# Kernel optimization log

Measured on AMD Instinct MI355X. Metric: run time of the kernel, lower is better.

Reference implementation:

```python
import jax, jax.numpy as jnp
import numpy as np

RES = 128            # occupancy grid resolution per axis
HIDDEN = 128         # MLP width
PE_POS = 10          # positional-encoding freqs for xyz
PE_DIR = 4           # positional-encoding freqs for viewdirs
S_MAX = 192          # max marching steps per ray
STEP = 0.027         # render_step_size (~aabb diagonal / S_MAX)
ERT = 1e-4           # early_stop_eps (transmittance threshold)
AABB_MIN = -1.5
AABB_MAX = 1.5
WHITE_BKGD = 1.0     # white_bkgd=True


def _posenc(x, L):
    # x: [..., 3] -> [..., 3 + 6L]
    freqs = 2.0 ** jnp.arange(L, dtype=x.dtype)
    xb = x[..., None, :] * freqs[:, None]                 # [..., L, 3]
    enc = jnp.concatenate([jnp.sin(xb), jnp.cos(xb)], axis=-1)  # [..., L, 6]
    return jnp.concatenate([x, enc.reshape(x.shape[:-1] + (-1,))], axis=-1)


def setup_inputs() -> dict:
    key = jax.random.key(0)
    ks = jax.random.split(key, 8)
    B, N = 1, 2048
    # camera origins on a sphere of radius 2.5 outside the aabb, rays aimed near the center
    o = jax.random.normal(ks[0], (B, N, 3), dtype=jnp.float32)
    o = o / jnp.linalg.norm(o, axis=-1, keepdims=True) * 2.5
    target = jax.random.normal(ks[1], (B, N, 3), dtype=jnp.float32) * 0.3
    d = target - o
    d = d / jnp.linalg.norm(d, axis=-1, keepdims=True)
    occ_grid = jax.random.bernoulli(ks[2], 0.3, (RES, RES, RES))
    din_pos = 3 + 6 * PE_POS   # 63
    din_dir = 3 + 6 * PE_DIR   # 27
    sc = lambda n: 1.0 / np.sqrt(n)
    W0 = jax.random.normal(ks[3], (din_pos, HIDDEN), dtype=jnp.float32) * sc(din_pos)
    W1 = jax.random.normal(ks[4], (HIDDEN, HIDDEN), dtype=jnp.float32) * sc(HIDDEN)
    w_sigma = jax.random.normal(ks[5], (HIDDEN, 1), dtype=jnp.float32) * sc(HIDDEN)
    W2 = jax.random.normal(ks[6], (HIDDEN + din_dir, HIDDEN), dtype=jnp.float32) * sc(HIDDEN)
    w_rgb = jax.random.normal(ks[7], (HIDDEN, 3), dtype=jnp.float32) * sc(HIDDEN)
    return {"rays_o": o, "viewdirs": d, "occ_grid": occ_grid,
            "W0": W0, "W1": W1, "w_sigma": w_sigma, "W2": W2, "w_rgb": w_rgb}


def reference(rays_o, viewdirs, occ_grid, W0, W1, w_sigma, W2, w_rgb):
    B, N, _ = rays_o.shape
    o = rays_o.reshape(-1, 3)          # [R, 3]
    d = viewdirs.reshape(-1, 3)        # [R, 3]
    R = o.shape[0]
    # ray / aabb intersection
    inv_d = 1.0 / jnp.where(jnp.abs(d) < 1e-9, 1e-9, d)
    t0 = (AABB_MIN - o) * inv_d
    t1 = (AABB_MAX - o) * inv_d
    t_near = jnp.maximum(jnp.max(jnp.minimum(t0, t1), axis=-1), 0.0)  # [R]
    t_far = jnp.min(jnp.maximum(t0, t1), axis=-1)                     # [R]
    # fixed-step marching (padded to S_MAX, masked) == nerfacc sampling with occ grid
    i = jnp.arange(S_MAX, dtype=rays_o.dtype)
    t_start = t_near[:, None] + STEP * i[None, :]   # [R, S]
    t_end = t_start + STEP
    t_mid = t_start + 0.5 * STEP
    inside = (t_mid < t_far[:, None]) & ((t_far > t_near)[:, None])
    pts = o[:, None, :] + d[:, None, :] * t_mid[..., None]  # [R, S, 3]
    # occupancy lookup (skip empty cells)
    gidx = jnp.clip(((pts - AABB_MIN) / (AABB_MAX - AABB_MIN) * RES).astype(jnp.int32), 0, RES - 1)
    occ = occ_grid[gidx[..., 0], gidx[..., 1], gidx[..., 2]]  # [R, S] bool
    mask = inside & occ
    # NeRF MLP (rgb_alpha_fn): sigma from pos, rgb from pos feature + viewdir
    pe_p = _posenc(pts.reshape(-1, 3), PE_POS)                               # [RS, 63]
    pe_d = _posenc(jnp.broadcast_to(d[:, None, :], pts.shape).reshape(-1, 3), PE_DIR)  # [RS, 27]
    h = jax.nn.relu(pe_p @ W0)
    h = jax.nn.relu(h @ W1)
    sigma = (h @ w_sigma).reshape(R, S_MAX)
    h2 = jax.nn.relu(jnp.concatenate([h, pe_d], axis=-1) @ W2)
    rgb = jax.nn.sigmoid(h2 @ w_rgb).reshape(R, S_MAX, 3)
    # alpha compositing (nerfacc.rendering) with early termination
    delta = t_end - t_start
    alpha = (1.0 - jnp.exp(-jax.nn.relu(sigma) * delta)) * mask.astype(sigma.dtype)
    trans = jnp.cumprod(1.0 - alpha + 1e-10, axis=-1)
    T = jnp.concatenate([jnp.ones((R, 1), alpha.dtype), trans[:, :-1]], axis=-1)  # exclusive
    T = T * (T > ERT).astype(T.dtype)  # early ray termination
    w = T * alpha                      # [R, S]
    rgb_map = jnp.einsum('rs,rsc->rc', w, rgb)
    opacity = jnp.sum(w, axis=-1, keepdims=True)
    depth = jnp.sum(w * t_mid, axis=-1, keepdims=True)
    rgb_map = rgb_map + (1.0 - opacity) * WHITE_BKGD
    return (rgb_map.reshape(B, N, 3), depth.reshape(B, N, 1), opacity.reshape(B, N, 1))
```

## Files before the change

### kernel.cpp

```cpp
#include <hip/hip_runtime.h>
#include <stdint.h>

#define NRAYS 2048
#define SMAX  192
#define RESG  128
#define STEPF 0.027f
#define ERTF  1e-4f
#define CAP   (NRAYS * SMAX)

typedef __attribute__((ext_vector_type(8)))  short bf16x8;
typedef __attribute__((ext_vector_type(16))) float f32x16;

__device__ __forceinline__ uint32_t f2b(float x) {
    uint32_t u = __builtin_bit_cast(uint32_t, x);
    return (u + 0x7fffu + ((u >> 16) & 1u)) >> 16;
}
__device__ __forceinline__ uint32_t bpack(float lo, float hi) {
    return f2b(lo) | (f2b(hi) << 16);
}

__device__ __forceinline__ void ray_aabb(float ox, float oy, float oz,
                                         float dx, float dy, float dz,
                                         float& tn, float& tf) {
    float ix = 1.0f / ((fabsf(dx) < 1e-9f) ? 1e-9f : dx);
    float iy = 1.0f / ((fabsf(dy) < 1e-9f) ? 1e-9f : dy);
    float iz = 1.0f / ((fabsf(dz) < 1e-9f) ? 1e-9f : dz);
    float t0x = (-1.5f - ox) * ix, t1x = (1.5f - ox) * ix;
    float t0y = (-1.5f - oy) * iy, t1y = (1.5f - oy) * iy;
    float t0z = (-1.5f - oz) * iz, t1z = (1.5f - oz) * iz;
    float tnx = fminf(t0x, t1x), tfx = fmaxf(t0x, t1x);
    float tny = fminf(t0y, t1y), tfy = fmaxf(t0y, t1y);
    float tnz = fminf(t0z, t1z), tfz = fmaxf(t0z, t1z);
    tn = fmaxf(fmaxf(fmaxf(tnx, tny), tnz), 0.0f);
    tf = fminf(fminf(tfx, tfy), tfz);
}

__global__ void k_prep(const float* __restrict__ W0, const float* __restrict__ W1,
                       const float* __restrict__ W2, uint32_t* __restrict__ wf) {
    int b = blockIdx.x;
    int g = b >> 2, oc = b & 3;
    int lane = threadIdx.x;
    int out = oc * 32 + (lane & 31);
    const float* W; int kbase, Klim;
    if (g < 4)       { W = W0; kbase = g * 16;        Klim = 63;  }
    else if (g < 12) { W = W1; kbase = (g - 4) * 16;  Klim = 128; }
    else             { W = W2; kbase = (g - 12) * 16; Klim = 155; }
    uint32_t d[4];
    #pragma unroll
    for (int h = 0; h < 4; ++h) {
        int k0 = kbase + ((lane >> 5) << 3) + h * 2;
        float lo = (k0     < Klim) ? W[(size_t)k0 * 128 + out]       : 0.0f;
        float hi = (k0 + 1 < Klim) ? W[(size_t)(k0 + 1) * 128 + out] : 0.0f;
        d[h] = bpack(lo, hi);
    }
    ((uint4*)wf)[b * 64 + lane] = make_uint4(d[0], d[1], d[2], d[3]);
}

__global__ __launch_bounds__(256) void k_count(
        const float* __restrict__ ro, const float* __restrict__ rd,
        const int* __restrict__ occ,
        int* __restrict__ rayCount, unsigned long long* __restrict__ masks) {
    int r = blockIdx.x * 4 + (threadIdx.x >> 6);
    int lane = threadIdx.x & 63;
    float ox = ro[r*3+0], oy = ro[r*3+1], oz = ro[r*3+2];
    float dx = rd[r*3+0], dy = rd[r*3+1], dz = rd[r*3+2];
    float tn, tf;
    ray_aabb(ox, oy, oz, dx, dy, dz, tn, tf);
    int cnt = 0;
    #pragma unroll
    for (int c = 0; c < 3; ++c) {
        int s = c * 64 + lane;
        float t_mid = (tn + STEPF * (float)s) + 0.5f * STEPF;
        bool inside = (t_mid < tf) && (tf > tn);
        bool act = false;
        if (inside) {
            float px = ox + dx * t_mid;
            float py = oy + dy * t_mid;
            float pz = oz + dz * t_mid;
            int gx = min(max((int)((px + 1.5f) / 3.0f * 128.0f), 0), RESG - 1);
            int gy = min(max((int)((py + 1.5f) / 3.0f * 128.0f), 0), RESG - 1);
            int gz = min(max((int)((pz + 1.5f) / 3.0f * 128.0f), 0), RESG - 1);
            act = occ[(gx * RESG + gy) * RESG + gz] != 0;
        }
        unsigned long long mb = __ballot(act);
        if (lane == 0) masks[r * 3 + c] = mb;
        cnt += __popcll(mb);
    }
    if (lane == 0) rayCount[r] = cnt;
}

__global__ __launch_bounds__(1024) void k_scan(
        const int* __restrict__ rayCount, int* __restrict__ rayOff,
        int* __restrict__ cnt_total) {
    __shared__ int wsum[16];
    int tid = threadIdx.x;
    int a = rayCount[2 * tid], b = rayCount[2 * tid + 1];
    int s = a + b;
    int lane = tid & 63, w = tid >> 6;
    int v = s;
    #pragma unroll
    for (int off = 1; off < 64; off <<= 1) {
        int t = __shfl_up(v, off);
        if (lane >= off) v += t;
    }
    if (lane == 63) wsum[w] = v;
    __syncthreads();
    if (tid < 16) {
        int x = wsum[tid];
        #pragma unroll
        for (int off = 1; off < 16; off <<= 1) {
            int t = __shfl_up(x, off, 16);
            if (tid >= off) x += t;
        }
        wsum[tid] = x;
    }
    __syncthreads();
    int wbase = (w == 0) ? 0 : wsum[w - 1];
    int incl = wbase + v;
    int excl = incl - s;
    rayOff[2 * tid]     = excl;
    rayOff[2 * tid + 1] = excl + a;
    if (tid == 1023) cnt_total[0] = incl;
}

__global__ __launch_bounds__(256) void k_fill(
        const float* __restrict__ ro, const float* __restrict__ rd,
        const int* __restrict__ rayOff, const unsigned long long* __restrict__ masks,
        int2* __restrict__ ids, float4* __restrict__ pos) {
    int r = blockIdx.x * 4 + (threadIdx.x >> 6);
    int lane = threadIdx.x & 63;
    float ox = ro[r*3+0], oy = ro[r*3+1], oz = ro[r*3+2];
    float dx = rd[r*3+0], dy = rd[r*3+1], dz = rd[r*3+2];
    float tn, tf;
    ray_aabb(ox, oy, oz, dx, dy, dz, tn, tf);
    int base = rayOff[r];
    #pragma unroll
    for (int c = 0; c < 3; ++c) {
        unsigned long long m = masks[r * 3 + c];
        if ((m >> lane) & 1ull) {
            int within = __popcll(m & ((1ull << lane) - 1ull));
            int s = c * 64 + lane;
            float t_mid = (tn + STEPF * (float)s) + 0.5f * STEPF;
            float px = ox + dx * t_mid;
            float py = oy + dy * t_mid;
            float pz = oz + dz * t_mid;
            ids[base + within] = make_int2(r, s);
            pos[base + within] = make_float4(px, py, pz, t_mid);
        }
        base += __popcll(m);
    }
}

__global__ __launch_bounds__(512) void k_mlp(
        const uint32_t* __restrict__ wfrag, const float* __restrict__ wsig,
        const float* __restrict__ wrgb, const float* __restrict__ vd,
        const int* __restrict__ cnt, const int2* __restrict__ ids,
        const float4* __restrict__ pos, float4* __restrict__ rgba) {
    __shared__ __align__(16) short actA[64 * 128];
    __shared__ __align__(16) short bufB[64 * 256];
    __shared__ float4 sPos[64];
    __shared__ int    sRay[64];
    __shared__ float  sV[128];
    __shared__ float  sR[384];

    const int tid  = threadIdx.x;
    const int wave = tid >> 6;
    const int lane = tid & 63;
    const int oc   = wave & 3;
    const int sc   = wave >> 2;
    const int lo5  = lane & 31;
    const int hi5  = lane >> 5;

    if (tid < 128) sV[tid] = wsig[tid];
    if (tid >= 128 && tid < 512) sR[tid - 128] = wrgb[tid - 128];

    bf16x8 wf[22];
    {
        const uint4* src = (const uint4*)wfrag;
        #pragma unroll
        for (int g = 0; g < 22; ++g) {
            uint4 v = src[(g * 4 + oc) * 64 + lane];
            wf[g] = __builtin_bit_cast(bf16x8, v);
        }
    }

    const int total  = *cnt;
    const int ntiles = (total + 63) >> 6;
    const int mrow   = sc * 32 + lo5;
    const int rswz   = (mrow & 15) << 4;

    for (int t = blockIdx.x; t < ntiles; t += gridDim.x) {
        const int base = t << 6;
        __syncthreads();
        if (tid < 64) {
            int gi = base + tid;
            if (gi < total) { sRay[tid] = ids[gi].x; sPos[tid] = pos[gi]; }
            else            { sRay[tid] = 0; sPos[tid] = make_float4(0.f,0.f,0.f,0.f); }
        }
        __syncthreads();

        {
            int m = tid >> 3, p = tid & 7;
            float4 P = sPos[m];
            int swz = (m & 15) << 4;
            uint32_t dw[4];
            #pragma unroll
            for (int jp = 0; jp < 4; ++jp) {
                float v[2];
                #pragma unroll
                for (int q = 0; q < 2; ++q) {
                    int c = p * 8 + jp * 2 + q;
                    float val;
                    if (c < 3)        val = (c == 0) ? P.x : ((c == 1) ? P.y : P.z);
                    else if (c >= 63) val = 0.0f;
                    else {
                        int cc = c - 3, l = cc / 6, jj = cc - 6 * l;
                        int a3 = (jj >= 3) ? jj - 3 : jj;
                        float comp = (a3 == 0) ? P.x : ((a3 == 1) ? P.y : P.z);
                        float arg = comp * (float)(1 << l);
                        val = (jj < 3) ? __sinf(arg) : __cosf(arg);
                    }
                    v[q] = val;
                }
                dw[jp] = bpack(v[0], v[1]);
            }
            *(uint4*)((char*)actA + m * 256 + ((p * 16) ^ swz)) = make_uint4(dw[0], dw[1], dw[2], dw[3]);
            if (p < 4) {
                int ray = sRay[m];
                float Dx = vd[ray*3+0], Dy = vd[ray*3+1], Dz = vd[ray*3+2];
                #pragma unroll
                for (int jp = 0; jp < 4; ++jp) {
                    float v[2];
                    #pragma unroll
                    for (int q = 0; q < 2; ++q) {
                        int c = p * 8 + jp * 2 + q;
                        float val;
                        if (c < 3)        val = (c == 0) ? Dx : ((c == 1) ? Dy : Dz);
                        else if (c >= 27) val = 0.0f;
                        else {
                            int cc = c - 3, l = cc / 6, jj = cc - 6 * l;
                            int a3 = (jj >= 3) ? jj - 3 : jj;
                            float comp = (a3 == 0) ? Dx : ((a3 == 1) ? Dy : Dz);
                            float arg = comp * (float)(1 << l);
                            val = (jj < 3) ? __sinf(arg) : __cosf(arg);
                        }
                        v[q] = val;
                    }
                    dw[jp] = bpack(v[0], v[1]);
                }
                *(uint4*)((char*)bufB + m * 512 + ((256 + p * 16) ^ swz)) = make_uint4(dw[0], dw[1], dw[2], dw[3]);
            }
        }
        __syncthreads();

        {
            f32x16 acc = {};
            #pragma unroll
            for (int kb = 0; kb < 4; ++kb) {
                bf16x8 bf = *(const bf16x8*)((const char*)actA + mrow * 256 + ((kb * 32 + (hi5 << 4)) ^ rswz));
                acc = __builtin_amdgcn_mfma_f32_32x32x16_bf16(wf[kb], bf, acc, 0, 0, 0);
            }
            #pragma unroll
            for (int g = 0; g < 4; ++g) {
                int outb = (oc * 32 + g * 8 + (hi5 << 2)) * 2;
                uint32_t d0 = bpack(fmaxf(acc[g*4+0], 0.f), fmaxf(acc[g*4+1], 0.f));
                uint32_t d1 = bpack(fmaxf(acc[g*4+2], 0.f), fmaxf(acc[g*4+3], 0.f));
                *(uint2*)((char*)bufB + mrow * 512 + (outb ^ rswz)) = make_uint2(d0, d1);
            }
        }
        __syncthreads();

        {
            f32x16 acc = {};
            #pragma unroll
            for (int kb = 0; kb < 8; ++kb) {
                bf16x8 bf = *(const bf16x8*)((const char*)bufB + mrow * 512 + ((kb * 32 + (hi5 << 4)) ^ rswz));
                acc = __builtin_amdgcn_mfma_f32_32x32x16_bf16(wf[4 + kb], bf, acc, 0, 0, 0);
            }
            #pragma unroll
            for (int g = 0; g < 4; ++g) {
                int outb = (oc * 32 + g * 8 + (hi5 << 2)) * 2;
                uint32_t d0 = bpack(fmaxf(acc[g*4+0], 0.f), fmaxf(acc[g*4+1], 0.f));
                uint32_t d1 = bpack(fmaxf(acc[g*4+2], 0.f), fmaxf(acc[g*4+3], 0.f));
                *(uint2*)((char*)actA + mrow * 256 + (outb ^ rswz)) = make_uint2(d0, d1);
            }
        }
        __syncthreads();

        {
            f32x16 acc = {};
            #pragma unroll
            for (int kb = 0; kb < 8; ++kb) {
                bf16x8 bf = *(const bf16x8*)((const char*)actA + mrow * 256 + ((kb * 32 + (hi5 << 4)) ^ rswz));
                acc = __builtin_amdgcn_mfma_f32_32x32x16_bf16(wf[12 + kb], bf, acc, 0, 0, 0);
            }
            #pragma unroll
            for (int kb = 8; kb < 10; ++kb) {
                bf16x8 bf = *(const bf16x8*)((const char*)bufB + mrow * 512 + ((kb * 32 + (hi5 << 4)) ^ rswz));
                acc = __builtin_amdgcn_mfma_f32_32x32x16_bf16(wf[12 + kb], bf, acc, 0, 0, 0);
            }
            #pragma unroll
            for (int g = 0; g < 4; ++g) {
                int outb = (oc * 32 + g * 8 + (hi5 << 2)) * 2;
                uint32_t d0 = bpack(fmaxf(acc[g*4+0], 0.f), fmaxf(acc[g*4+1], 0.f));
                uint32_t d1 = bpack(fmaxf(acc[g*4+2], 0.f), fmaxf(acc[g*4+3], 0.f));
                *(uint2*)((char*)bufB + mrow * 512 + (outb ^ rswz)) = make_uint2(d0, d1);
            }
        }
        __syncthreads();

        {
            int m = tid >> 3, p = tid & 7;
            int swz = (m & 15) << 4;
            float sp = 0.f, r0 = 0.f, r1 = 0.f, r2 = 0.f;
            #pragma unroll
            for (int hh = 0; hh < 2; ++hh) {
                uint4 q = *(const uint4*)((const char*)actA + m * 256 + ((p * 32 + hh * 16) ^ swz));
                uint32_t w[4] = {q.x, q.y, q.z, q.w};
                #pragma unroll
                for (int e = 0; e < 4; ++e) {
                    int j = p * 16 + hh * 8 + e * 2;
                    float a0 = __builtin_bit_cast(float, w[e] << 16);
                    float a1 = __builtin_bit_cast(float, w[e] & 0xffff0000u);
                    sp = fmaf(a0, sV[j], sp);
                    sp = fmaf(a1, sV[j + 1], sp);
                }
            }
            #pragma unroll
            for (int hh = 0; hh < 2; ++hh) {
                uint4 q = *(const uint4*)((const char*)bufB + m * 512 + ((p * 32 + hh * 16) ^ swz));
                uint32_t w[4] = {q.x, q.y, q.z, q.w};
                #pragma unroll
                for (int e = 0; e < 4; ++e) {
                    int j = p * 16 + hh * 8 + e * 2;
                    float a0 = __builtin_bit_cast(float, w[e] << 16);
                    float a1 = __builtin_bit_cast(float, w[e] & 0xffff0000u);
                    r0 = fmaf(a0, sR[j*3+0], r0); r1 = fmaf(a0, sR[j*3+1], r1); r2 = fmaf(a0, sR[j*3+2], r2);
                    r0 = fmaf(a1, sR[(j+1)*3+0], r0); r1 = fmaf(a1, sR[(j+1)*3+1], r1); r2 = fmaf(a1, sR[(j+1)*3+2], r2);
                }
            }
            #pragma unroll
            for (int off = 1; off < 8; off <<= 1) {
                sp += __shfl_xor(sp, off);
                r0 += __shfl_xor(r0, off);
                r1 += __shfl_xor(r1, off);
                r2 += __shfl_xor(r2, off);
            }
            if (p == 0 && (base + m) < total) {
                float alpha = 1.0f - __expf(-fmaxf(sp, 0.0f) * STEPF);
                float c0 = 1.0f / (1.0f + __expf(-r0));
                float c1 = 1.0f / (1.0f + __expf(-r1));
                float c2 = 1.0f / (1.0f + __expf(-r2));
                rgba[base + m] = make_float4(c0, c1, c2, alpha);
            }
        }
    }
}

__global__ __launch_bounds__(256) void k_render(
        const int* __restrict__ rayOff, const int* __restrict__ rayCount,
        const float4* __restrict__ rgba, const float* __restrict__ posw,
        float* __restrict__ out) {
    int r = blockIdx.x * 4 + (threadIdx.x >> 6);
    int lane = threadIdx.x & 63;
    int off = rayOff[r], cnt = rayCount[r];
    float T_run = 1.0f;
    float cr = 0.f, cg = 0.f, cb = 0.f, opa = 0.f, dep = 0.f;
    for (int j = 0; j < cnt; j += 64) {
        int idx = j + lane;
        float4 f = make_float4(0.f, 0.f, 0.f, 0.f);
        float tmid = 0.f;
        if (idx < cnt) {
            f = rgba[off + idx];
            tmid = posw[(size_t)(off + idx) * 4 + 3];
        }
        float p = (1.0f - f.w) + 1e-10f;
        #pragma unroll
        for (int o = 1; o < 64; o <<= 1) {
            float v = __shfl_up(p, o);
            if (lane >= o) p *= v;
        }
        float pprev = __shfl_up(p, 1);
        float Texc = (lane == 0) ? T_run : T_run * pprev;
        Texc = (Texc > ERTF) ? Texc : 0.0f;
        float w = Texc * f.w;
        cr += w * f.x; cg += w * f.y; cb += w * f.z;
        opa += w; dep += w * tmid;
        T_run *= __shfl(p, 63);
        if (T_run <= ERTF) break;
    }
    #pragma unroll
    for (int o = 32; o; o >>= 1) {
        cr  += __shfl_xor(cr, o);
        cg  += __shfl_xor(cg, o);
        cb  += __shfl_xor(cb, o);
        opa += __shfl_xor(opa, o);
        dep += __shfl_xor(dep, o);
    }
    if (lane == 0) {
        out[r * 3 + 0] = cr + (1.0f - opa);
        out[r * 3 + 1] = cg + (1.0f - opa);
        out[r * 3 + 2] = cb + (1.0f - opa);
        out[NRAYS * 3 + r] = dep;
        out[NRAYS * 4 + r] = opa;
    }
}

extern "C" void kernel_launch(void* const* d_in, const int* in_sizes, int n_in,
                              void* d_out, int out_size, void* d_ws, size_t ws_size,
                              hipStream_t stream) {
    const float* ro   = (const float*)d_in[0];
    const float* rd   = (const float*)d_in[1];
    const int*   occ  = (const int*)d_in[2];
    const float* W0   = (const float*)d_in[3];
    const float* W1   = (const float*)d_in[4];
    const float* wsig = (const float*)d_in[5];
    const float* W2   = (const float*)d_in[6];
    const float* wrgb = (const float*)d_in[7];
    float* out = (float*)d_out;

    char* ws = (char*)d_ws;
    int*                cnt_total = (int*)ws;
    int*                rayCount  = (int*)(ws + 16);
    int*                rayOff    = (int*)(ws + 8208);
    unsigned long long* masks     = (unsigned long long*)(ws + 16400);
    int2*               ids       = (int2*)(ws + 65552);
    float4*             pos       = (float4*)(ws + 65552 + (size_t)CAP * 8);
    float4*             rgba      = (float4*)(ws + 65552 + (size_t)CAP * 24);
    uint32_t*           wfrag     = (uint32_t*)(ws + 65552 + (size_t)CAP * 40);

    k_prep  <<<88, 64, 0, stream>>>(W0, W1, W2, wfrag);
    k_count <<<NRAYS / 4, 256, 0, stream>>>(ro, rd, occ, rayCount, masks);
    k_scan  <<<1, 1024, 0, stream>>>(rayCount, rayOff, cnt_total);
    k_fill  <<<NRAYS / 4, 256, 0, stream>>>(ro, rd, rayOff, masks, ids, pos);
    k_mlp   <<<1024, 512, 0, stream>>>(wfrag, wsig, wrgb, rd, cnt_total, ids, pos, rgba);
    k_render<<<NRAYS / 4, 256, 0, stream>>>(rayOff, rayCount, rgba, (const float*)pos, out);
}
```

Measured before the change: 119.6 us.

## Enlarge MLP tile to 128 samples, merge weight prep into count kernel

The MLP kernel now processes 128 samples per tile instead of 64. Each wave issues two MFMAs per weight fragment, so every register-resident weight is reused across twice as many rows, and the grid drops from 1024 to 256 blocks. The weight-packing kernel is merged into the count kernel as extra blocks to remove one launch, and the sample id buffer shrinks from int2 to a single int. The trade-off is that LDS use per block roughly doubles, which may lower occupancy, and with fewer, larger tiles the load may balance less evenly across CUs.

```diff
diff --git a/kernel.cpp b/kernel.cpp
--- a/kernel.cpp
+++ b/kernel.cpp
@@ -35,32 +35,36 @@
     tf = fminf(fminf(tfx, tfy), tfz);
 }
 
-__global__ void k_prep(const float* __restrict__ W0, const float* __restrict__ W1,
-                       const float* __restrict__ W2, uint32_t* __restrict__ wf) {
-    int b = blockIdx.x;
-    int g = b >> 2, oc = b & 3;
-    int lane = threadIdx.x;
-    int out = oc * 32 + (lane & 31);
-    const float* W; int kbase, Klim;
-    if (g < 4)       { W = W0; kbase = g * 16;        Klim = 63;  }
-    else if (g < 12) { W = W1; kbase = (g - 4) * 16;  Klim = 128; }
-    else             { W = W2; kbase = (g - 12) * 16; Klim = 155; }
-    uint32_t d[4];
-    #pragma unroll
-    for (int h = 0; h < 4; ++h) {
-        int k0 = kbase + ((lane >> 5) << 3) + h * 2;
-        float lo = (k0     < Klim) ? W[(size_t)k0 * 128 + out]       : 0.0f;
-        float hi = (k0 + 1 < Klim) ? W[(size_t)(k0 + 1) * 128 + out] : 0.0f;
-        d[h] = bpack(lo, hi);
-    }
-    ((uint4*)wf)[b * 64 + lane] = make_uint4(d[0], d[1], d[2], d[3]);
-}
-
-__global__ __launch_bounds__(256) void k_count(
+__global__ __launch_bounds__(256) void k_count_prep(
         const float* __restrict__ ro, const float* __restrict__ rd,
         const int* __restrict__ occ,
-        int* __restrict__ rayCount, unsigned long long* __restrict__ masks) {
-    int r = blockIdx.x * 4 + (threadIdx.x >> 6);
+        const float* __restrict__ W0, const float* __restrict__ W1,
+        const float* __restrict__ W2,
+        int* __restrict__ rayCount, unsigned long long* __restrict__ masks,
+        uint32_t* __restrict__ wfrag) {
+    int b = blockIdx.x;
+    if (b >= NRAYS / 4) {
+        int pb = b - NRAYS / 4;
+        int lane = threadIdx.x;
+        if (lane >= 64) return;
+        int g = pb >> 2, oc = pb & 3;
+        int out = oc * 32 + (lane & 31);
+        const float* W; int kbase, Klim;
+        if (g < 4)       { W = W0; kbase = g * 16;        Klim = 63;  }
+        else if (g < 12) { W = W1; kbase = (g - 4) * 16;  Klim = 128; }
+        else             { W = W2; kbase = (g - 12) * 16; Klim = 155; }
+        uint32_t d[4];
+        #pragma unroll
+        for (int h = 0; h < 4; ++h) {
+            int k0 = kbase + ((lane >> 5) << 3) + h * 2;
+            float lo = (k0     < Klim) ? W[(size_t)k0 * 128 + out]       : 0.0f;
+            float hi = (k0 + 1 < Klim) ? W[(size_t)(k0 + 1) * 128 + out] : 0.0f;
+            d[h] = bpack(lo, hi);
+        }
+        ((uint4*)wfrag)[pb * 64 + lane] = make_uint4(d[0], d[1], d[2], d[3]);
+        return;
+    }
+    int r = b * 4 + (threadIdx.x >> 6);
     int lane = threadIdx.x & 63;
     float ox = ro[r*3+0], oy = ro[r*3+1], oz = ro[r*3+2];
     float dx = rd[r*3+0], dy = rd[r*3+1], dz = rd[r*3+2];
@@ -126,7 +130,7 @@
 __global__ __launch_bounds__(256) void k_fill(
         const float* __restrict__ ro, const float* __restrict__ rd,
         const int* __restrict__ rayOff, const unsigned long long* __restrict__ masks,
-        int2* __restrict__ ids, float4* __restrict__ pos) {
+        int* __restrict__ rayid, float4* __restrict__ pos) {
     int r = blockIdx.x * 4 + (threadIdx.x >> 6);
     int lane = threadIdx.x & 63;
     float ox = ro[r*3+0], oy = ro[r*3+1], oz = ro[r*3+2];
@@ -144,7 +148,7 @@
             float px = ox + dx * t_mid;
             float py = oy + dy * t_mid;
             float pz = oz + dz * t_mid;
-            ids[base + within] = make_int2(r, s);
+            rayid[base + within] = r;
             pos[base + within] = make_float4(px, py, pz, t_mid);
         }
         base += __popcll(m);
@@ -154,12 +158,12 @@
 __global__ __launch_bounds__(512) void k_mlp(
         const uint32_t* __restrict__ wfrag, const float* __restrict__ wsig,
         const float* __restrict__ wrgb, const float* __restrict__ vd,
-        const int* __restrict__ cnt, const int2* __restrict__ ids,
+        const int* __restrict__ cnt, const int* __restrict__ rayid,
         const float4* __restrict__ pos, float4* __restrict__ rgba) {
-    __shared__ __align__(16) short actA[64 * 128];
-    __shared__ __align__(16) short bufB[64 * 256];
-    __shared__ float4 sPos[64];
-    __shared__ int    sRay[64];
+    __shared__ __align__(16) short actA[128 * 128];
+    __shared__ __align__(16) short bufB[128 * 256];
+    __shared__ float4 sPos[128];
+    __shared__ int    sRay[128];
     __shared__ float  sV[128];
     __shared__ float  sR[384];
 
@@ -185,49 +189,53 @@
     }
 
     const int total  = *cnt;
-    const int ntiles = (total + 63) >> 6;
-    const int mrow   = sc * 32 + lo5;
+    const int ntiles = (total + 127) >> 7;
+    const int mrow   = sc * 64 + lo5;
     const int rswz   = (mrow & 15) << 4;
 
     for (int t = blockIdx.x; t < ntiles; t += gridDim.x) {
-        const int base = t << 6;
-        __syncthreads();
-        if (tid < 64) {
+        const int base = t << 7;
+        __syncthreads();
+        if (tid < 128) {
             int gi = base + tid;
-            if (gi < total) { sRay[tid] = ids[gi].x; sPos[tid] = pos[gi]; }
+            if (gi < total) { sRay[tid] = rayid[gi]; sPos[tid] = pos[gi]; }
             else            { sRay[tid] = 0; sPos[tid] = make_float4(0.f,0.f,0.f,0.f); }
         }
         __syncthreads();
 
         {
-            int m = tid >> 3, p = tid & 7;
+            int m = tid >> 2, p = tid & 3;
             float4 P = sPos[m];
             int swz = (m & 15) << 4;
-            uint32_t dw[4];
-            #pragma unroll
-            for (int jp = 0; jp < 4; ++jp) {
-                float v[2];
+            #pragma unroll
+            for (int half = 0; half < 2; ++half) {
+                uint32_t dw[4];
                 #pragma unroll
-                for (int q = 0; q < 2; ++q) {
-                    int c = p * 8 + jp * 2 + q;
-                    float val;
-                    if (c < 3)        val = (c == 0) ? P.x : ((c == 1) ? P.y : P.z);
-                    else if (c >= 63) val = 0.0f;
-                    else {
-                        int cc = c - 3, l = cc / 6, jj = cc - 6 * l;
-                        int a3 = (jj >= 3) ? jj - 3 : jj;
-                        float comp = (a3 == 0) ? P.x : ((a3 == 1) ? P.y : P.z);
-                        float arg = comp * (float)(1 << l);
-                        val = (jj < 3) ? __sinf(arg) : __cosf(arg);
+                for (int jp = 0; jp < 4; ++jp) {
+                    float v[2];
+                    #pragma unroll
+                    for (int q = 0; q < 2; ++q) {
+                        int c = p * 16 + half * 8 + jp * 2 + q;
+                        float val;
+                        if (c < 3)        val = (c == 0) ? P.x : ((c == 1) ? P.y : P.z);
+                        else if (c >= 63) val = 0.0f;
+                        else {
+                            int cc = c - 3, l = cc / 6, jj = cc - 6 * l;
+                            int a3 = (jj >= 3) ? jj - 3 : jj;
+                            float comp = (a3 == 0) ? P.x : ((a3 == 1) ? P.y : P.z);
+                            float arg = comp * (float)(1 << l);
+                            val = (jj < 3) ? __sinf(arg) : __cosf(arg);
+                        }
+                        v[q] = val;
                     }
-                    v[q] = val;
+                    dw[jp] = bpack(v[0], v[1]);
                 }
-                dw[jp] = bpack(v[0], v[1]);
-            }
-            *(uint4*)((char*)actA + m * 256 + ((p * 16) ^ swz)) = make_uint4(dw[0], dw[1], dw[2], dw[3]);
-            if (p < 4) {
+                *(uint4*)((char*)actA + m * 256 + ((p * 32 + half * 16) ^ swz)) = make_uint4(dw[0], dw[1], dw[2], dw[3]);
+            }
+            {
                 int ray = sRay[m];
                 float Dx = vd[ray*3+0], Dy = vd[ray*3+1], Dz = vd[ray*3+2];
+                uint32_t dw[4];
                 #pragma unroll
                 for (int jp = 0; jp < 4; ++jp) {
                     float v[2];
@@ -254,72 +262,93 @@
         __syncthreads();
 
         {
-            f32x16 acc = {};
+            f32x16 a0 = {}, a1 = {};
             #pragma unroll
             for (int kb = 0; kb < 4; ++kb) {
-                bf16x8 bf = *(const bf16x8*)((const char*)actA + mrow * 256 + ((kb * 32 + (hi5 << 4)) ^ rswz));
-                acc = __builtin_amdgcn_mfma_f32_32x32x16_bf16(wf[kb], bf, acc, 0, 0, 0);
+                int cb = (kb * 32 + (hi5 << 4)) ^ rswz;
+                bf16x8 b0 = *(const bf16x8*)((const char*)actA + mrow * 256 + cb);
+                bf16x8 b1 = *(const bf16x8*)((const char*)actA + (mrow + 32) * 256 + cb);
+                a0 = __builtin_amdgcn_mfma_f32_32x32x16_bf16(wf[kb], b0, a0, 0, 0, 0);
+                a1 = __builtin_amdgcn_mfma_f32_32x32x16_bf16(wf[kb], b1, a1, 0, 0, 0);
             }
             #pragma unroll
             for (int g = 0; g < 4; ++g) {
                 int outb = (oc * 32 + g * 8 + (hi5 << 2)) * 2;
-                uint32_t d0 = bpack(fmaxf(acc[g*4+0], 0.f), fmaxf(acc[g*4+1], 0.f));
-                uint32_t d1 = bpack(fmaxf(acc[g*4+2], 0.f), fmaxf(acc[g*4+3], 0.f));
-                *(uint2*)((char*)bufB + mrow * 512 + (outb ^ rswz)) = make_uint2(d0, d1);
+                *(uint2*)((char*)bufB + mrow * 512 + (outb ^ rswz)) =
+                    make_uint2(bpack(fmaxf(a0[g*4+0],0.f), fmaxf(a0[g*4+1],0.f)),
+                               bpack(fmaxf(a0[g*4+2],0.f), fmaxf(a0[g*4+3],0.f)));
+                *(uint2*)((char*)bufB + (mrow + 32) * 512 + (outb ^ rswz)) =
+                    make_uint2(bpack(fmaxf(a1[g*4+0],0.f), fmaxf(a1[g*4+1],0.f)),
+                               bpack(fmaxf(a1[g*4+2],0.f), fmaxf(a1[g*4+3],0.f)));
             }
         }
         __syncthreads();
 
         {
-            f32x16 acc = {};
+            f32x16 a0 = {}, a1 = {};
             #pragma unroll
             for (int kb = 0; kb < 8; ++kb) {
-                bf16x8 bf = *(const bf16x8*)((const char*)bufB + mrow * 512 + ((kb * 32 + (hi5 << 4)) ^ rswz));
-                acc = __builtin_amdgcn_mfma_f32_32x32x16_bf16(wf[4 + kb], bf, acc, 0, 0, 0);
+                int cb = (kb * 32 + (hi5 << 4)) ^ rswz;
+                bf16x8 b0 = *(const bf16x8*)((const char*)bufB + mrow * 512 + cb);
+                bf16x8 b1 = *(const bf16x8*)((const char*)bufB + (mrow + 32) * 512 + cb);
+                a0 = __builtin_amdgcn_mfma_f32_32x32x16_bf16(wf[4 + kb], b0, a0, 0, 0, 0);
+                a1 = __builtin_amdgcn_mfma_f32_32x32x16_bf16(wf[4 + kb], b1, a1, 0, 0, 0);
             }
             #pragma unroll
             for (int g = 0; g < 4; ++g) {
                 int outb = (oc * 32 + g * 8 + (hi5 << 2)) * 2;
-                uint32_t d0 = bpack(fmaxf(acc[g*4+0], 0.f), fmaxf(acc[g*4+1], 0.f));
-                uint32_t d1 = bpack(fmaxf(acc[g*4+2], 0.f), fmaxf(acc[g*4+3], 0.f));
-                *(uint2*)((char*)actA + mrow * 256 + (outb ^ rswz)) = make_uint2(d0, d1);
+                *(uint2*)((char*)actA + mrow * 256 + (outb ^ rswz)) =
+                    make_uint2(bpack(fmaxf(a0[g*4+0],0.f), fmaxf(a0[g*4+1],0.f)),
+                               bpack(fmaxf(a0[g*4+2],0.f), fmaxf(a0[g*4+3],0.f)));
+                *(uint2*)((char*)actA + (mrow + 32) * 256 + (outb ^ rswz)) =
+                    make_uint2(bpack(fmaxf(a1[g*4+0],0.f), fmaxf(a1[g*4+1],0.f)),
+                               bpack(fmaxf(a1[g*4+2],0.f), fmaxf(a1[g*4+3],0.f)));
             }
         }
         __syncthreads();
 
         {
-            f32x16 acc = {};
+            f32x16 a0 = {}, a1 = {};
             #pragma unroll
             for (int kb = 0; kb < 8; ++kb) {
-                bf16x8 bf = *(const bf16x8*)((const char*)actA + mrow * 256 + ((kb * 32 + (hi5 << 4)) ^ rswz));
-                acc = __builtin_amdgcn_mfma_f32_32x32x16_bf16(wf[12 + kb], bf, acc, 0, 0, 0);
+                int cb = (kb * 32 + (hi5 << 4)) ^ rswz;
+                bf16x8 b0 = *(const bf16x8*)((const char*)actA + mrow * 256 + cb);
+                bf16x8 b1 = *(const bf16x8*)((const char*)actA + (mrow + 32) * 256 + cb);
+                a0 = __builtin_amdgcn_mfma_f32_32x32x16_bf16(wf[12 + kb], b0, a0, 0, 0, 0);
+                a1 = __builtin_amdgcn_mfma_f32_32x32x16_bf16(wf[12 + kb], b1, a1, 0, 0, 0);
             }
             #pragma unroll
             for (int kb = 8; kb < 10; ++kb) {
-                bf16x8 bf = *(const bf16x8*)((const char*)bufB + mrow * 512 + ((kb * 32 + (hi5 << 4)) ^ rswz));
-                acc = __builtin_amdgcn_mfma_f32_32x32x16_bf16(wf[12 + kb], bf, acc, 0, 0, 0);
+                int cb = (kb * 32 + (hi5 << 4)) ^ rswz;
+                bf16x8 b0 = *(const bf16x8*)((const char*)bufB + mrow * 512 + cb);
+                bf16x8 b1 = *(const bf16x8*)((const char*)bufB + (mrow + 32) * 512 + cb);
+                a0 = __builtin_amdgcn_mfma_f32_32x32x16_bf16(wf[12 + kb], b0, a0, 0, 0, 0);
+                a1 = __builtin_amdgcn_mfma_f32_32x32x16_bf16(wf[12 + kb], b1, a1, 0, 0, 0);
             }
             #pragma unroll
             for (int g = 0; g < 4; ++g) {
                 int outb = (oc * 32 + g * 8 + (hi5 << 2)) * 2;
-                uint32_t d0 = bpack(fmaxf(acc[g*4+0], 0.f), fmaxf(acc[g*4+1], 0.f));
-                uint32_t d1 = bpack(fmaxf(acc[g*4+2], 0.f), fmaxf(acc[g*4+3], 0.f));
-                *(uint2*)((char*)bufB + mrow * 512 + (outb ^ rswz)) = make_uint2(d0, d1);
+                *(uint2*)((char*)bufB + mrow * 512 + (outb ^ rswz)) =
+                    make_uint2(bpack(fmaxf(a0[g*4+0],0.f), fmaxf(a0[g*4+1],0.f)),
+                               bpack(fmaxf(a0[g*4+2],0.f), fmaxf(a0[g*4+3],0.f)));
+                *(uint2*)((char*)bufB + (mrow + 32) * 512 + (outb ^ rswz)) =
+                    make_uint2(bpack(fmaxf(a1[g*4+0],0.f), fmaxf(a1[g*4+1],0.f)),
+                               bpack(fmaxf(a1[g*4+2],0.f), fmaxf(a1[g*4+3],0.f)));
             }
         }
         __syncthreads();
 
         {
-            int m = tid >> 3, p = tid & 7;
+            int m = tid >> 2, p = tid & 3;
             int swz = (m & 15) << 4;
             float sp = 0.f, r0 = 0.f, r1 = 0.f, r2 = 0.f;
             #pragma unroll
-            for (int hh = 0; hh < 2; ++hh) {
-                uint4 q = *(const uint4*)((const char*)actA + m * 256 + ((p * 32 + hh * 16) ^ swz));
+            for (int hh = 0; hh < 4; ++hh) {
+                uint4 q = *(const uint4*)((const char*)actA + m * 256 + ((p * 64 + hh * 16) ^ swz));
                 uint32_t w[4] = {q.x, q.y, q.z, q.w};
                 #pragma unroll
                 for (int e = 0; e < 4; ++e) {
-                    int j = p * 16 + hh * 8 + e * 2;
+                    int j = p * 32 + hh * 8 + e * 2;
                     float a0 = __builtin_bit_cast(float, w[e] << 16);
                     float a1 = __builtin_bit_cast(float, w[e] & 0xffff0000u);
                     sp = fmaf(a0, sV[j], sp);
@@ -327,12 +356,12 @@
                 }
             }
             #pragma unroll
-            for (int hh = 0; hh < 2; ++hh) {
-                uint4 q = *(const uint4*)((const char*)bufB + m * 512 + ((p * 32 + hh * 16) ^ swz));
+            for (int hh = 0; hh < 4; ++hh) {
+                uint4 q = *(const uint4*)((const char*)bufB + m * 512 + ((p * 64 + hh * 16) ^ swz));
                 uint32_t w[4] = {q.x, q.y, q.z, q.w};
                 #pragma unroll
                 for (int e = 0; e < 4; ++e) {
-                    int j = p * 16 + hh * 8 + e * 2;
+                    int j = p * 32 + hh * 8 + e * 2;
                     float a0 = __builtin_bit_cast(float, w[e] << 16);
                     float a1 = __builtin_bit_cast(float, w[e] & 0xffff0000u);
                     r0 = fmaf(a0, sR[j*3+0], r0); r1 = fmaf(a0, sR[j*3+1], r1); r2 = fmaf(a0, sR[j*3+2], r2);
@@ -340,7 +369,7 @@
                 }
             }
             #pragma unroll
-            for (int off = 1; off < 8; off <<= 1) {
+            for (int off = 1; off < 4; off <<= 1) {
                 sp += __shfl_xor(sp, off);
                 r0 += __shfl_xor(r0, off);
                 r1 += __shfl_xor(r1, off);
@@ -424,15 +453,15 @@
     int*                rayCount  = (int*)(ws + 16);
     int*                rayOff    = (int*)(ws + 8208);
     unsigned long long* masks     = (unsigned long long*)(ws + 16400);
-    int2*               ids       = (int2*)(ws + 65552);
+    int*                rayid     = (int*)(ws + 65552);
     float4*             pos       = (float4*)(ws + 65552 + (size_t)CAP * 8);
     float4*             rgba      = (float4*)(ws + 65552 + (size_t)CAP * 24);
     uint32_t*           wfrag     = (uint32_t*)(ws + 65552 + (size_t)CAP * 40);
 
-    k_prep  <<<88, 64, 0, stream>>>(W0, W1, W2, wfrag);
-    k_count <<<NRAYS / 4, 256, 0, stream>>>(ro, rd, occ, rayCount, masks);
+    k_count_prep <<<NRAYS / 4 + 88, 256, 0, stream>>>(ro, rd, occ, W0, W1, W2,
+                                                      rayCount, masks, wfrag);
     k_scan  <<<1, 1024, 0, stream>>>(rayCount, rayOff, cnt_total);
-    k_fill  <<<NRAYS / 4, 256, 0, stream>>>(ro, rd, rayOff, masks, ids, pos);
-    k_mlp   <<<1024, 512, 0, stream>>>(wfrag, wsig, wrgb, rd, cnt_total, ids, pos, rgba);
+    k_fill  <<<NRAYS / 4, 256, 0, stream>>>(ro, rd, rayOff, masks, rayid, pos);
+    k_mlp   <<<256, 512, 0, stream>>>(wfrag, wsig, wrgb, rd, cnt_total, rayid, pos, rgba);
     k_render<<<NRAYS / 4, 256, 0, stream>>>(rayOff, rayCount, rgba, (const float*)pos, out);
 }
```

New measurement: 114.2 us. 1.05x faster.
